# Kernel optimization log

Hardware: AMD Instinct MI355X
Metric: run time of the kernel (lower is better)

Reference implementation:

```python
import jax, jax.numpy as jnp
import numpy as np

TEMP = 0.7
ALPHA_ADV = 1.0
BETA_BAND = 0.5
BAND_L = 0.05
BAND_H = 0.2
W_HEUR = 0.5
W_LEAR = 0.5


def setup_inputs() -> dict:
    key = jax.random.key(0)
    ks = jax.random.split(key, 6)
    B, Sn, C, H, W = 2, 5, 64, 192, 192
    hid = 64
    return {
        "S": jax.random.normal(ks[0], (B, C, H, W), jnp.float32),
        "T": jax.random.normal(ks[1], (B, Sn, C, H, W), jnp.float32),
        "adapt_w": jax.random.normal(ks[2], (Sn, C, C), jnp.float32) / np.sqrt(C).astype(np.float32),
        "adapt_b": jnp.zeros((Sn, C), jnp.float32),
        "r_w1": jax.random.normal(ks[3], (hid, Sn * C * 3), jnp.float32) * 0.05,
        "r_b1": jnp.zeros((hid,), jnp.float32),
        "r_w2": jax.random.normal(ks[4], (Sn, hid), jnp.float32) * 0.05,
        "r_b2": jnp.zeros((Sn,), jnp.float32),
        "ema_mu": jnp.zeros((1, Sn, C, 1, 1), jnp.float32),
        "ema_sigma": jnp.ones((1, Sn, C, 1, 1), jnp.float32),
        "ema_proxy": jnp.zeros((1, Sn, 1, 1, 1), jnp.float32),
    }


def reference(S, T, adapt_w, adapt_b, r_w1, r_b1, r_w2, r_b2, ema_mu, ema_sigma, ema_proxy):
    B, Sn, C, H, W = T.shape
    bias = adapt_b[None, :, :, None, None]
    # per-sweep 1x1 conv == per-sweep channel matmul
    T_adapt = jnp.einsum('sdc,bschw->bsdhw', adapt_w, T) + bias          # [B,S,C,H,W]
    S_rep = jnp.einsum('sdc,bchw->bsdhw', adapt_w, S) + bias             # [B,S,C,H,W]
    Tz = (T_adapt - ema_mu) / ema_sigma
    Sz = (S_rep - ema_mu) / ema_sigma
    delta = Tz - Sz
    proxy = jnp.mean(delta * delta, axis=2, keepdims=True)               # [B,S,1,H,W]
    cur = jnp.mean(proxy, axis=(0, 3, 4), keepdims=True)                 # [1,S,1,1,1]
    # heuristic score (gamma_ucb = 0 -> no UCB term)
    impr = jax.lax.stop_gradient(ema_proxy - cur)
    adv = impr - jnp.mean(impr, axis=1, keepdims=True)
    below = jnp.maximum(BAND_L - cur, 0.0)
    above = jnp.maximum(cur - BAND_H, 0.0)
    band = -(below * below + above * above)
    score = ALPHA_ADV * adv + BETA_BAND * band                           # [1,S,1,1,1]
    score_heur = jnp.broadcast_to(score, proxy.shape)[:, :, 0]           # [B,S,H,W]
    # learned router: concat along channel of each sweep then 1x1 MLP
    x = jnp.concatenate([Sz, Tz, delta], axis=2).reshape(B, Sn * 3 * C, H, W)
    h = jax.nn.relu(jnp.einsum('oi,bihw->bohw', r_w1, x) + r_b1[None, :, None, None])
    score_learn = jnp.einsum('oi,bihw->bohw', r_w2, h) + r_b2[None, :, None, None]
    logits = W_HEUR * score_heur + W_LEAR * score_learn                  # [B,S,H,W]
    weights = jax.nn.softmax(logits / TEMP, axis=1)                      # soft gating over sweeps
    return weights
```

## Files before the change

### kernel.cpp

```cpp
#include <hip/hip_runtime.h>
#include <math.h>

#define HWSZ 36864
#define NTILE 576
#define NBLK 1152

typedef short bf16x8 __attribute__((ext_vector_type(8)));
typedef float f32x16 __attribute__((ext_vector_type(16)));
typedef unsigned int u32x4 __attribute__((ext_vector_type(4)));

__device__ __forceinline__ unsigned short f2bf(float x) {
    unsigned u = __float_as_uint(x);
    return (unsigned short)((u + 0x7fffu + ((u >> 16) & 1u)) >> 16);
}

__global__ void pre_dmat(const float* __restrict__ aw, const float* __restrict__ sigma,
                         float* __restrict__ Dmat) {
    int idx = blockIdx.x * 256 + threadIdx.x;
    if (idx < 20480) {
        int sd = idx >> 6;
        Dmat[idx] = aw[idx] / sigma[sd];
    }
}

__global__ void pre_weights(const float* __restrict__ rw1, const float* __restrict__ rb1,
                            const float* __restrict__ ab, const float* __restrict__ mu,
                            const float* __restrict__ sigma, const float* __restrict__ Dmat,
                            float* __restrict__ MT, float* __restrict__ MSp,
                            float* __restrict__ c1) {
    int idx = blockIdx.x * 256 + threadIdx.x;
    if (idx < 20480) {
        int s = idx / 4096, r = idx % 4096, o = r >> 6, c = r & 63;
        float sum = 0.f;
        const float* wp = rw1 + o * 960 + s * 192;
        const float* D  = Dmat + s * 4096 + c;
        #pragma unroll 8
        for (int d = 0; d < 64; ++d)
            sum = fmaf(wp[64 + d] + wp[128 + d], D[d * 64], sum);
        MT[idx] = sum;
    } else if (idx < 24576) {
        int k = idx - 20480;
        int o = k >> 6, c = k & 63;
        float sum = 0.f;
        for (int s = 0; s < 5; ++s) {
            const float* wp = rw1 + o * 960 + s * 192;
            const float* D  = Dmat + s * 4096 + c;
            #pragma unroll 8
            for (int d = 0; d < 64; ++d)
                sum = fmaf(wp[d] + wp[64 + d], D[d * 64], sum);
        }
        MSp[k] = sum;
    } else if (idx < 24640) {
        int o = idx - 24576;
        float sum = rb1[o];
        for (int s = 0; s < 5; ++s) {
            const float* wp = rw1 + o * 960 + s * 192;
            #pragma unroll 8
            for (int d = 0; d < 64; ++d) {
                int sd = s * 64 + d;
                sum = fmaf(wp[d] + wp[64 + d], (ab[sd] - mu[sd]) / sigma[sd], sum);
            }
        }
        c1[o] = sum;
    }
}

__global__ void pre_pack(const float* __restrict__ Dmat, const float* __restrict__ MT,
                         const float* __restrict__ MSp,
                         unsigned short* __restrict__ AfragW,
                         unsigned short* __restrict__ AfragSp) {
    int i = blockIdx.x * 256 + threadIdx.x;
    if (i < 40960) {
        int s = i / 8192, rem = i % 8192;
        int r = rem / 2048, rem2 = rem % 2048;
        int t = rem2 / 512, q = rem2 % 512;
        int l = q >> 3, e = q & 7;
        int R = 32 * r + (l & 31);
        int k = 16 * t + 8 * (l >> 5) + e;
        float v = (R < 64) ? Dmat[s * 4096 + R * 64 + k] : MT[s * 4096 + (R - 64) * 64 + k];
        AfragW[i] = f2bf(v);
    } else if (i < 45056) {
        int j = i - 40960;
        int r = j / 2048, rem2 = j % 2048;
        int t = rem2 / 512, q = rem2 % 512;
        int l = q >> 3, e = q & 7;
        float v = MSp[(32 * r + (l & 31)) * 64 + 16 * t + 8 * (l >> 5) + e];
        AfragSp[j] = f2bf(v);
    }
}

__global__ __launch_bounds__(256) void fused_main(
        const float* __restrict__ S, const float* __restrict__ T,
        const unsigned short* __restrict__ AfragW, const unsigned short* __restrict__ AfragSp,
        const float* __restrict__ c1, const float* __restrict__ rw2, const float* __restrict__ rb2,
        float* __restrict__ slearn, float* __restrict__ partial) {
    __shared__ __align__(16) unsigned short Xb[4096];
    __shared__ __align__(16) unsigned short Sb[4096];
    __shared__ float hbuf[64][64];
    __shared__ float wred[5][2];
    __shared__ float c1s[64];

    const int tid  = threadIdx.x;
    const int lane = tid & 63;
    const int w    = tid >> 6;
    const int blk  = blockIdx.x;
    const int b    = blk / NTILE;
    const int pix0 = (blk % NTILE) * 64;

    const int hi = lane >> 5;
    const int px = lane & 31;

    if (tid < 64) c1s[tid] = c1[tid];

    {
        const int pg = tid & 7, c0 = tid >> 3;
        for (int it = 0; it < 2; ++it) {
            int c = c0 + 32 * it;
            const float* Sp = S + ((size_t)(b * 64 + c)) * HWSZ + pix0 + pg * 8;
            float4 s0 = *(const float4*)Sp;
            float4 s1 = *(const float4*)(Sp + 4);
            u32x4 o;
            o.x = f2bf(s0.x) | ((unsigned)f2bf(s0.y) << 16);
            o.y = f2bf(s0.z) | ((unsigned)f2bf(s0.w) << 16);
            o.z = f2bf(s1.x) | ((unsigned)f2bf(s1.y) << 16);
            o.w = f2bf(s1.z) | ((unsigned)f2bf(s1.w) << 16);
            *(u32x4*)&Sb[c * 64 + pg * 8] = o;
        }
    }
    __syncthreads();

    auto stage_row = [&](int s, int c, int pg) {
        const float* Tp = T + ((size_t)((b * 5 + s) * 64 + c)) * HWSZ + pix0 + pg * 8;
        const float* Sp = S + ((size_t)(b * 64 + c)) * HWSZ + pix0 + pg * 8;
        float4 t0 = *(const float4*)Tp;
        float4 t1 = *(const float4*)(Tp + 4);
        float4 s0 = *(const float4*)Sp;
        float4 s1 = *(const float4*)(Sp + 4);
        u32x4 o;
        o.x = f2bf(t0.x - s0.x) | ((unsigned)f2bf(t0.y - s0.y) << 16);
        o.y = f2bf(t0.z - s0.z) | ((unsigned)f2bf(t0.w - s0.w) << 16);
        o.z = f2bf(t1.x - s1.x) | ((unsigned)f2bf(t1.y - s1.y) << 16);
        o.w = f2bf(t1.z - s1.z) | ((unsigned)f2bf(t1.w - s1.w) << 16);
        *(u32x4*)&Xb[c * 64 + pg * 8] = o;
    };

    auto run_gemm = [&](const unsigned short* afr, int fragblk, const unsigned short* lds,
                        f32x16& accA, f32x16& accB) {
        const bf16x8* ap = reinterpret_cast<const bf16x8*>(afr) + (size_t)fragblk * 256 + lane;
        bf16x8 Af[4];
        #pragma unroll
        for (int kt = 0; kt < 4; ++kt) Af[kt] = ap[kt * 64];
        #pragma unroll
        for (int kt = 0; kt < 4; ++kt) {
            bf16x8 Bq;
            int base = (kt * 16 + hi * 8) * 64 + px;
            #pragma unroll
            for (int e = 0; e < 8; ++e) Bq[e] = (short)lds[base + e * 64];
            accA = __builtin_amdgcn_mfma_f32_32x32x16_bf16(Af[kt], Bq, accA, 0, 0, 0);
        }
        #pragma unroll
        for (int kt = 0; kt < 4; ++kt) {
            bf16x8 Bq;
            int base = (kt * 16 + hi * 8) * 64 + px + 32;
            #pragma unroll
            for (int e = 0; e < 8; ++e) Bq[e] = (short)lds[base + e * 64];
            accB = __builtin_amdgcn_mfma_f32_32x32x16_bf16(Af[kt], Bq, accB, 0, 0, 0);
        }
    };

    f32x16 acc0, acc1;
    #pragma unroll
    for (int i = 0; i < 16; ++i) { acc0[i] = 0.f; acc1[i] = 0.f; }

    if (w < 2) {
        run_gemm(AfragSp, w, Sb, acc0, acc1);
        #pragma unroll
        for (int i = 0; i < 16; ++i) {
            int row = (i & 3) + 8 * (i >> 2) + 4 * hi + 32 * w;
            hbuf[row][px]      = acc0[i];
            hbuf[row][px + 32] = acc1[i];
        }
    } else {
        int t2 = tid - 128;
        int pg = t2 & 7, cb = t2 >> 3;
        for (int it = 0; it < 4; ++it) stage_row(0, cb + 16 * it, pg);
    }
    __syncthreads();

    for (int s = 0; s < 5; ++s) {
        if (w < 2) {
            #pragma unroll
            for (int i = 0; i < 16; ++i) { acc0[i] = 0.f; acc1[i] = 0.f; }
        }
        run_gemm(AfragW, s * 4 + w, Xb, acc0, acc1);
        if (w < 2) {
            float sq = 0.f;
            #pragma unroll
            for (int i = 0; i < 16; ++i) {
                sq = fmaf(acc0[i], acc0[i], sq);
                sq = fmaf(acc1[i], acc1[i], sq);
            }
            #pragma unroll
            for (int m = 1; m < 64; m <<= 1) sq += __shfl_xor(sq, m, 64);
            if (lane == 0) wred[s][w] = sq;
        }
        __syncthreads();
        if (s < 4) {
            int pg = tid & 7, c0 = tid >> 3;
            stage_row(s + 1, c0, pg);
            stage_row(s + 1, c0 + 32, pg);
            __syncthreads();
        }
    }

    if (w >= 2) {
        #pragma unroll
        for (int i = 0; i < 16; ++i) {
            int row = (i & 3) + 8 * (i >> 2) + 4 * hi + 32 * (w - 2);
            float v0 = hbuf[row][px]      + acc0[i] + c1s[row];
            float v1 = hbuf[row][px + 32] + acc1[i] + c1s[row];
            hbuf[row][px]      = fmaxf(v0, 0.f);
            hbuf[row][px + 32] = fmaxf(v1, 0.f);
        }
    }
    __syncthreads();

    {
        int p = tid & 63;
        for (int sp = w; sp < 5; sp += 4) {
            float sum = rb2[sp];
            #pragma unroll 8
            for (int o = 0; o < 64; ++o) sum = fmaf(rw2[sp * 64 + o], hbuf[o][p], sum);
            slearn[((size_t)(b * 5 + sp)) * HWSZ + pix0 + p] = sum;
        }
    }
    if (tid < 5) partial[blk * 5 + tid] = wred[tid][0] + wred[tid][1];
}

__global__ void score_kernel(const float* __restrict__ partial,
                             const float* __restrict__ ema_proxy,
                             float* __restrict__ scoreBuf) {
    __shared__ float red[256];
    __shared__ float cur[5];
    int tid = threadIdx.x;
    for (int s = 0; s < 5; ++s) {
        float sum = 0.f;
        for (int i = tid; i < NBLK; i += 256) sum += partial[i * 5 + s];
        red[tid] = sum;
        __syncthreads();
        for (int off = 128; off > 0; off >>= 1) {
            if (tid < off) red[tid] += red[tid + off];
            __syncthreads();
        }
        if (tid == 0) cur[s] = red[0] * (1.0f / (64.0f * 2.0f * HWSZ));
        __syncthreads();
    }
    if (tid == 0) {
        float impr[5]; float m = 0.f;
        for (int s = 0; s < 5; ++s) { impr[s] = ema_proxy[s] - cur[s]; m += impr[s]; }
        m *= 0.2f;
        for (int s = 0; s < 5; ++s) {
            float adv = impr[s] - m;
            float c = cur[s];
            float below = fmaxf(0.05f - c, 0.f);
            float above = fmaxf(c - 0.2f, 0.f);
            float band = -(below * below + above * above);
            scoreBuf[s] = 1.0f * adv + 0.5f * band;
        }
    }
}

__global__ void softmax_kernel(const float* __restrict__ slearn,
                               const float* __restrict__ scoreBuf,
                               float* __restrict__ out) {
    int i = blockIdx.x * 256 + threadIdx.x;
    if (i >= 2 * HWSZ) return;
    int b = i / HWSZ, p = i % HWSZ;
    float l[5];
    float mx = -1e30f;
    #pragma unroll
    for (int s = 0; s < 5; ++s) {
        float v = (0.5f * scoreBuf[s] + 0.5f * slearn[((size_t)(b * 5 + s)) * HWSZ + p]) / 0.7f;
        l[s] = v;
        mx = fmaxf(mx, v);
    }
    float sum = 0.f;
    #pragma unroll
    for (int s = 0; s < 5; ++s) { l[s] = expf(l[s] - mx); sum += l[s]; }
    float inv = 1.0f / sum;
    #pragma unroll
    for (int s = 0; s < 5; ++s) out[((size_t)(b * 5 + s)) * HWSZ + p] = l[s] * inv;
}

extern "C" void kernel_launch(void* const* d_in, const int* in_sizes, int n_in,
                              void* d_out, int out_size, void* d_ws, size_t ws_size,
                              hipStream_t stream) {
    const float* S   = (const float*)d_in[0];
    const float* T   = (const float*)d_in[1];
    const float* aw  = (const float*)d_in[2];
    const float* ab  = (const float*)d_in[3];
    const float* rw1 = (const float*)d_in[4];
    const float* rb1 = (const float*)d_in[5];
    const float* rw2 = (const float*)d_in[6];
    const float* rb2 = (const float*)d_in[7];
    const float* mu  = (const float*)d_in[8];
    const float* sg  = (const float*)d_in[9];
    const float* ep  = (const float*)d_in[10];

    float* ws = (float*)d_ws;
    float* c1f      = ws;
    float* scoreBuf = ws + 64;
    float* partial  = ws + 72;
    unsigned short* AfragW  = (unsigned short*)(ws + 5832);
    unsigned short* AfragSp = (unsigned short*)(ws + 26312);
    float* slearn   = ws + 28360;
    float* Dmat     = ws + 28360;
    float* MT       = ws + 48840;
    float* MSp      = ws + 69320;
    float* out = (float*)d_out;

    pre_dmat<<<80, 256, 0, stream>>>(aw, sg, Dmat);
    pre_weights<<<97, 256, 0, stream>>>(rw1, rb1, ab, mu, sg, Dmat, MT, MSp, c1f);
    pre_pack<<<176, 256, 0, stream>>>(Dmat, MT, MSp, AfragW, AfragSp);
    fused_main<<<NBLK, 256, 0, stream>>>(S, T, AfragW, AfragSp, c1f, rw2, rb2, slearn, partial);
    score_kernel<<<1, 256, 0, stream>>>(partial, ep, scoreBuf);
    softmax_kernel<<<288, 256, 0, stream>>>(slearn, scoreBuf, out);
}
```

Baseline: 69.29 us.

## Restructure fused kernel: 128-pixel tiles, register-prefetched T, double-buffered LDS, register MLP

Each block now covers 128 pixels instead of 64, so half as many blocks are launched. Each wave owns a 32-pixel column and runs both the delta and hidden GEMMs for all four M-tiles, which keeps the hidden accumulators in registers across sweeps. S is read once and kept in registers as bf16, while the next sweep's T is prefetched into registers and written to an alternating LDS buffer with an XOR swizzle, removing one barrier per sweep and the repeated S reloads. The final 64-to-5 projection is done from registers with a cross-half shuffle instead of through an LDS hidden buffer. The cost is higher register pressure, fewer blocks for occupancy, and S being rounded to bf16 before the subtraction.

```diff
diff --git a/kernel.cpp b/kernel.cpp
--- a/kernel.cpp
+++ b/kernel.cpp
@@ -2,8 +2,9 @@
 #include <math.h>
 
 #define HWSZ 36864
-#define NTILE 576
-#define NBLK 1152
+#define NPIX 128
+#define NT2  288
+#define NBLK2 576
 
 typedef short bf16x8 __attribute__((ext_vector_type(8)));
 typedef float f32x16 __attribute__((ext_vector_type(16)));
@@ -94,147 +95,195 @@
         const unsigned short* __restrict__ AfragW, const unsigned short* __restrict__ AfragSp,
         const float* __restrict__ c1, const float* __restrict__ rw2, const float* __restrict__ rb2,
         float* __restrict__ slearn, float* __restrict__ partial) {
-    __shared__ __align__(16) unsigned short Xb[4096];
-    __shared__ __align__(16) unsigned short Sb[4096];
-    __shared__ float hbuf[64][64];
-    __shared__ float wred[5][2];
+    __shared__ __align__(16) unsigned short bufA[8192];
+    __shared__ __align__(16) unsigned short bufB[8192];
+    __shared__ float w2s[320];
     __shared__ float c1s[64];
+    __shared__ float rb2s[8];
+    __shared__ float wred[5][4];
 
     const int tid  = threadIdx.x;
     const int lane = tid & 63;
     const int w    = tid >> 6;
+    const int hi   = lane >> 5;
+    const int px   = lane & 31;
+    const int col  = (w << 5) + px;
+
     const int blk  = blockIdx.x;
-    const int b    = blk / NTILE;
-    const int pix0 = (blk % NTILE) * 64;
-
-    const int hi = lane >> 5;
-    const int px = lane & 31;
-
+    const int b    = blk / NT2;
+    const int pix0 = (blk % NT2) * NPIX;
+
+    for (int i = tid; i < 320; i += 256) w2s[i] = rw2[i];
     if (tid < 64) c1s[tid] = c1[tid];
+    if (tid < 5)  rb2s[tid] = rb2[tid];
+
+    const int pg = tid & 7;
+    const int c0 = tid >> 3;
+    const float* Sbase = S + ((size_t)b * 64) * HWSZ + pix0 + pg * 16;
+    const float* Tbase = T + ((size_t)(b * 5) * 64) * HWSZ + pix0 + pg * 16;
+
+    float4 sldr[8];
+    #pragma unroll
+    for (int r = 0; r < 2; ++r) {
+        const float* p = Sbase + (size_t)(c0 + 32 * r) * HWSZ;
+        #pragma unroll
+        for (int j = 0; j < 4; ++j) sldr[r * 4 + j] = *(const float4*)(p + 4 * j);
+    }
+    float4 tr[8];
+    #pragma unroll
+    for (int r = 0; r < 2; ++r) {
+        const float* p = Tbase + (size_t)(c0 + 32 * r) * HWSZ;
+        #pragma unroll
+        for (int j = 0; j < 4; ++j) tr[r * 4 + j] = *(const float4*)(p + 4 * j);
+    }
+
+    u32x4 sreg[4];
+    #pragma unroll
+    for (int r = 0; r < 2; ++r) {
+        const float4* v = sldr + 4 * r;
+        unsigned o[8];
+        #pragma unroll
+        for (int q = 0; q < 4; ++q) {
+            o[2 * q]     = (unsigned)f2bf(v[q].x) | ((unsigned)f2bf(v[q].y) << 16);
+            o[2 * q + 1] = (unsigned)f2bf(v[q].z) | ((unsigned)f2bf(v[q].w) << 16);
+        }
+        u32x4 o0, o1;
+        o0.x = o[0]; o0.y = o[1]; o0.z = o[2]; o0.w = o[3];
+        o1.x = o[4]; o1.y = o[5]; o1.z = o[6]; o1.w = o[7];
+        sreg[2 * r] = o0; sreg[2 * r + 1] = o1;
+        int c = c0 + 32 * r;
+        int flip = (c & 8) ? 32 : 0;
+        unsigned short* dst = &bufA[c * 128 + ((pg * 16) ^ flip)];
+        *(u32x4*)dst = o0;
+        *(u32x4*)(dst + 8) = o1;
+    }
+    __syncthreads();
+
+    auto writeX = [&](unsigned short* buf) {
+        #pragma unroll
+        for (int r = 0; r < 2; ++r) {
+            const float4* t = tr + 4 * r;
+            float f[16];
+            #pragma unroll
+            for (int q = 0; q < 4; ++q) {
+                f[4 * q] = t[q].x; f[4 * q + 1] = t[q].y;
+                f[4 * q + 2] = t[q].z; f[4 * q + 3] = t[q].w;
+            }
+            unsigned spv[8];
+            spv[0] = sreg[2 * r].x; spv[1] = sreg[2 * r].y; spv[2] = sreg[2 * r].z; spv[3] = sreg[2 * r].w;
+            spv[4] = sreg[2 * r + 1].x; spv[5] = sreg[2 * r + 1].y; spv[6] = sreg[2 * r + 1].z; spv[7] = sreg[2 * r + 1].w;
+            unsigned o[8];
+            #pragma unroll
+            for (int k = 0; k < 8; ++k) {
+                float slo = __uint_as_float(spv[k] << 16);
+                float shi = __uint_as_float(spv[k] & 0xffff0000u);
+                unsigned short xlo = f2bf(f[2 * k] - slo);
+                unsigned short xhi = f2bf(f[2 * k + 1] - shi);
+                o[k] = (unsigned)xlo | ((unsigned)xhi << 16);
+            }
+            u32x4 o0, o1;
+            o0.x = o[0]; o0.y = o[1]; o0.z = o[2]; o0.w = o[3];
+            o1.x = o[4]; o1.y = o[5]; o1.z = o[6]; o1.w = o[7];
+            int c = c0 + 32 * r;
+            int flip = (c & 8) ? 32 : 0;
+            unsigned short* dst = &buf[c * 128 + ((pg * 16) ^ flip)];
+            *(u32x4*)dst = o0;
+            *(u32x4*)(dst + 8) = o1;
+        }
+    };
+    auto loadT = [&](int s) {
+        #pragma unroll
+        for (int r = 0; r < 2; ++r) {
+            const float* p = Tbase + (size_t)(s * 64 + c0 + 32 * r) * HWSZ;
+            #pragma unroll
+            for (int j = 0; j < 4; ++j) tr[r * 4 + j] = *(const float4*)(p + 4 * j);
+        }
+    };
+
+    f32x16 h0, h1;
+    #pragma unroll
+    for (int i = 0; i < 16; ++i) { h0[i] = 0.f; h1[i] = 0.f; }
 
     {
-        const int pg = tid & 7, c0 = tid >> 3;
-        for (int it = 0; it < 2; ++it) {
-            int c = c0 + 32 * it;
-            const float* Sp = S + ((size_t)(b * 64 + c)) * HWSZ + pix0 + pg * 8;
-            float4 s0 = *(const float4*)Sp;
-            float4 s1 = *(const float4*)(Sp + 4);
-            u32x4 o;
-            o.x = f2bf(s0.x) | ((unsigned)f2bf(s0.y) << 16);
-            o.y = f2bf(s0.z) | ((unsigned)f2bf(s0.w) << 16);
-            o.z = f2bf(s1.x) | ((unsigned)f2bf(s1.y) << 16);
-            o.w = f2bf(s1.z) | ((unsigned)f2bf(s1.w) << 16);
-            *(u32x4*)&Sb[c * 64 + pg * 8] = o;
-        }
-    }
+        const bf16x8* ap = (const bf16x8*)AfragSp + lane;
+        #pragma unroll
+        for (int kt = 0; kt < 4; ++kt) {
+            int k0 = kt * 16 + hi * 8;
+            int flip = hi ? 32 : 0;
+            const unsigned short* bp = &bufA[k0 * 128 + (col ^ flip)];
+            bf16x8 Bq;
+            #pragma unroll
+            for (int e = 0; e < 8; ++e) Bq[e] = (short)bp[e * 128];
+            h0 = __builtin_amdgcn_mfma_f32_32x32x16_bf16(ap[(0 * 4 + kt) * 64], Bq, h0, 0, 0, 0);
+            h1 = __builtin_amdgcn_mfma_f32_32x32x16_bf16(ap[(1 * 4 + kt) * 64], Bq, h1, 0, 0, 0);
+        }
+    }
+    writeX(bufB);
+    loadT(1);
     __syncthreads();
 
-    auto stage_row = [&](int s, int c, int pg) {
-        const float* Tp = T + ((size_t)((b * 5 + s) * 64 + c)) * HWSZ + pix0 + pg * 8;
-        const float* Sp = S + ((size_t)(b * 64 + c)) * HWSZ + pix0 + pg * 8;
-        float4 t0 = *(const float4*)Tp;
-        float4 t1 = *(const float4*)(Tp + 4);
-        float4 s0 = *(const float4*)Sp;
-        float4 s1 = *(const float4*)(Sp + 4);
-        u32x4 o;
-        o.x = f2bf(t0.x - s0.x) | ((unsigned)f2bf(t0.y - s0.y) << 16);
-        o.y = f2bf(t0.z - s0.z) | ((unsigned)f2bf(t0.w - s0.w) << 16);
-        o.z = f2bf(t1.x - s1.x) | ((unsigned)f2bf(t1.y - s1.y) << 16);
-        o.w = f2bf(t1.z - s1.z) | ((unsigned)f2bf(t1.w - s1.w) << 16);
-        *(u32x4*)&Xb[c * 64 + pg * 8] = o;
-    };
-
-    auto run_gemm = [&](const unsigned short* afr, int fragblk, const unsigned short* lds,
-                        f32x16& accA, f32x16& accB) {
-        const bf16x8* ap = reinterpret_cast<const bf16x8*>(afr) + (size_t)fragblk * 256 + lane;
-        bf16x8 Af[4];
-        #pragma unroll
-        for (int kt = 0; kt < 4; ++kt) Af[kt] = ap[kt * 64];
+    #pragma unroll
+    for (int s = 0; s < 5; ++s) {
+        const unsigned short* cur = (s & 1) ? bufA : bufB;
+        unsigned short* nxt       = (s & 1) ? bufB : bufA;
+        const bf16x8* ap = (const bf16x8*)AfragW + (size_t)(s * 16) * 64 + lane;
+
+        f32x16 d0, d1;
+        #pragma unroll
+        for (int i = 0; i < 16; ++i) { d0[i] = 0.f; d1[i] = 0.f; }
+
         #pragma unroll
         for (int kt = 0; kt < 4; ++kt) {
+            int k0 = kt * 16 + hi * 8;
+            int flip = hi ? 32 : 0;
+            const unsigned short* bp = &cur[k0 * 128 + (col ^ flip)];
             bf16x8 Bq;
-            int base = (kt * 16 + hi * 8) * 64 + px;
-            #pragma unroll
-            for (int e = 0; e < 8; ++e) Bq[e] = (short)lds[base + e * 64];
-            accA = __builtin_amdgcn_mfma_f32_32x32x16_bf16(Af[kt], Bq, accA, 0, 0, 0);
-        }
-        #pragma unroll
-        for (int kt = 0; kt < 4; ++kt) {
-            bf16x8 Bq;
-            int base = (kt * 16 + hi * 8) * 64 + px + 32;
-            #pragma unroll
-            for (int e = 0; e < 8; ++e) Bq[e] = (short)lds[base + e * 64];
-            accB = __builtin_amdgcn_mfma_f32_32x32x16_bf16(Af[kt], Bq, accB, 0, 0, 0);
-        }
-    };
-
-    f32x16 acc0, acc1;
-    #pragma unroll
-    for (int i = 0; i < 16; ++i) { acc0[i] = 0.f; acc1[i] = 0.f; }
-
-    if (w < 2) {
-        run_gemm(AfragSp, w, Sb, acc0, acc1);
+            #pragma unroll
+            for (int e = 0; e < 8; ++e) Bq[e] = (short)bp[e * 128];
+            d0 = __builtin_amdgcn_mfma_f32_32x32x16_bf16(ap[(0 * 4 + kt) * 64], Bq, d0, 0, 0, 0);
+            d1 = __builtin_amdgcn_mfma_f32_32x32x16_bf16(ap[(1 * 4 + kt) * 64], Bq, d1, 0, 0, 0);
+            h0 = __builtin_amdgcn_mfma_f32_32x32x16_bf16(ap[(2 * 4 + kt) * 64], Bq, h0, 0, 0, 0);
+            h1 = __builtin_amdgcn_mfma_f32_32x32x16_bf16(ap[(3 * 4 + kt) * 64], Bq, h1, 0, 0, 0);
+        }
+        float sq = 0.f;
         #pragma unroll
         for (int i = 0; i < 16; ++i) {
-            int row = (i & 3) + 8 * (i >> 2) + 4 * hi + 32 * w;
-            hbuf[row][px]      = acc0[i];
-            hbuf[row][px + 32] = acc1[i];
-        }
-    } else {
-        int t2 = tid - 128;
-        int pg = t2 & 7, cb = t2 >> 3;
-        for (int it = 0; it < 4; ++it) stage_row(0, cb + 16 * it, pg);
-    }
-    __syncthreads();
-
-    for (int s = 0; s < 5; ++s) {
-        if (w < 2) {
-            #pragma unroll
-            for (int i = 0; i < 16; ++i) { acc0[i] = 0.f; acc1[i] = 0.f; }
-        }
-        run_gemm(AfragW, s * 4 + w, Xb, acc0, acc1);
-        if (w < 2) {
-            float sq = 0.f;
-            #pragma unroll
-            for (int i = 0; i < 16; ++i) {
-                sq = fmaf(acc0[i], acc0[i], sq);
-                sq = fmaf(acc1[i], acc1[i], sq);
-            }
-            #pragma unroll
-            for (int m = 1; m < 64; m <<= 1) sq += __shfl_xor(sq, m, 64);
-            if (lane == 0) wred[s][w] = sq;
+            sq = fmaf(d0[i], d0[i], sq);
+            sq = fmaf(d1[i], d1[i], sq);
+        }
+        #pragma unroll
+        for (int m = 1; m < 64; m <<= 1) sq += __shfl_xor(sq, m, 64);
+        if (lane == 0) wred[s][w] = sq;
+
+        if (s < 4) {
+            writeX(nxt);
+            if (s < 3) loadT(s + 2);
         }
         __syncthreads();
-        if (s < 4) {
-            int pg = tid & 7, c0 = tid >> 3;
-            stage_row(s + 1, c0, pg);
-            stage_row(s + 1, c0 + 32, pg);
-            __syncthreads();
-        }
-    }
-
-    if (w >= 2) {
+    }
+
+    if (tid < 5)
+        partial[blk * 5 + tid] = wred[tid][0] + wred[tid][1] + wred[tid][2] + wred[tid][3];
+
+    #pragma unroll
+    for (int i = 0; i < 16; ++i) {
+        int row0 = (i & 3) + 8 * (i >> 2) + 4 * hi;
+        h0[i] = fmaxf(h0[i] + c1s[row0], 0.f);
+        h1[i] = fmaxf(h1[i] + c1s[row0 + 32], 0.f);
+    }
+    #pragma unroll
+    for (int sp = 0; sp < 5; ++sp) {
+        float acc = 0.f;
         #pragma unroll
         for (int i = 0; i < 16; ++i) {
-            int row = (i & 3) + 8 * (i >> 2) + 4 * hi + 32 * (w - 2);
-            float v0 = hbuf[row][px]      + acc0[i] + c1s[row];
-            float v1 = hbuf[row][px + 32] + acc1[i] + c1s[row];
-            hbuf[row][px]      = fmaxf(v0, 0.f);
-            hbuf[row][px + 32] = fmaxf(v1, 0.f);
-        }
-    }
-    __syncthreads();
-
-    {
-        int p = tid & 63;
-        for (int sp = w; sp < 5; sp += 4) {
-            float sum = rb2[sp];
-            #pragma unroll 8
-            for (int o = 0; o < 64; ++o) sum = fmaf(rw2[sp * 64 + o], hbuf[o][p], sum);
-            slearn[((size_t)(b * 5 + sp)) * HWSZ + pix0 + p] = sum;
-        }
-    }
-    if (tid < 5) partial[blk * 5 + tid] = wred[tid][0] + wred[tid][1];
+            int row0 = (i & 3) + 8 * (i >> 2) + 4 * hi;
+            acc = fmaf(w2s[sp * 64 + row0], h0[i], acc);
+            acc = fmaf(w2s[sp * 64 + row0 + 32], h1[i], acc);
+        }
+        acc += __shfl_xor(acc, 32, 64);
+        if (lane < 32)
+            slearn[((size_t)(b * 5 + sp)) * HWSZ + pix0 + col] = acc + rb2s[sp];
+    }
 }
 
 __global__ void score_kernel(const float* __restrict__ partial,
@@ -245,7 +294,7 @@
     int tid = threadIdx.x;
     for (int s = 0; s < 5; ++s) {
         float sum = 0.f;
-        for (int i = tid; i < NBLK; i += 256) sum += partial[i * 5 + s];
+        for (int i = tid; i < NBLK2; i += 256) sum += partial[i * 5 + s];
         red[tid] = sum;
         __syncthreads();
         for (int off = 128; off > 0; off >>= 1) {
@@ -322,7 +371,7 @@
     pre_dmat<<<80, 256, 0, stream>>>(aw, sg, Dmat);
     pre_weights<<<97, 256, 0, stream>>>(rw1, rb1, ab, mu, sg, Dmat, MT, MSp, c1f);
     pre_pack<<<176, 256, 0, stream>>>(Dmat, MT, MSp, AfragW, AfragSp);
-    fused_main<<<NBLK, 256, 0, stream>>>(S, T, AfragW, AfragSp, c1f, rw2, rb2, slearn, partial);
+    fused_main<<<NBLK2, 256, 0, stream>>>(S, T, AfragW, AfragSp, c1f, rw2, rb2, slearn, partial);
     score_kernel<<<1, 256, 0, stream>>>(partial, ep, scoreBuf);
     softmax_kernel<<<288, 256, 0, stream>>>(slearn, scoreBuf, out);
 }
```

Result: slower. 78.58 us (+13.4%).

## Restructure fused kernel into single-wave 32-pixel tiles with register-resident operands

Applied to the files above, without the earlier changes.

The main kernel now uses one 64-thread wave per 32-pixel tile instead of a 256-thread block per 64-pixel tile. S and T are loaded straight from global memory into registers as MFMA B-operands, replacing the LDS staging buffers and block barriers. The hidden layer stays in accumulators, and the second layer is reduced with a shuffle. T loads for the next sweep are software-pipelined against the current GEMM, and pre_dmat is fused into pre_weights to remove a launch. The cost is strided scalar global loads with 32-pixel coalescing instead of float4 loads, higher register pressure, and twice as many partial sums.

```diff
diff --git a/kernel.cpp b/kernel.cpp
--- a/kernel.cpp
+++ b/kernel.cpp
@@ -2,8 +2,8 @@
 #include <math.h>
 
 #define HWSZ 36864
-#define NTILE 576
-#define NBLK 1152
+#define NWID 2304
+#define PXW  32
 
 typedef short bf16x8 __attribute__((ext_vector_type(8)));
 typedef float f32x16 __attribute__((ext_vector_type(16)));
@@ -14,29 +14,22 @@
     return (unsigned short)((u + 0x7fffu + ((u >> 16) & 1u)) >> 16);
 }
 
-__global__ void pre_dmat(const float* __restrict__ aw, const float* __restrict__ sigma,
-                         float* __restrict__ Dmat) {
+__global__ void pre_weights(const float* __restrict__ rw1, const float* __restrict__ rb1,
+                            const float* __restrict__ aw, const float* __restrict__ ab,
+                            const float* __restrict__ mu, const float* __restrict__ sg,
+                            float* __restrict__ Dmat, float* __restrict__ MT,
+                            float* __restrict__ MSp, float* __restrict__ c1) {
     int idx = blockIdx.x * 256 + threadIdx.x;
     if (idx < 20480) {
-        int sd = idx >> 6;
-        Dmat[idx] = aw[idx] / sigma[sd];
-    }
-}
-
-__global__ void pre_weights(const float* __restrict__ rw1, const float* __restrict__ rb1,
-                            const float* __restrict__ ab, const float* __restrict__ mu,
-                            const float* __restrict__ sigma, const float* __restrict__ Dmat,
-                            float* __restrict__ MT, float* __restrict__ MSp,
-                            float* __restrict__ c1) {
-    int idx = blockIdx.x * 256 + threadIdx.x;
-    if (idx < 20480) {
+        Dmat[idx] = aw[idx] / sg[idx >> 6];
         int s = idx / 4096, r = idx % 4096, o = r >> 6, c = r & 63;
         float sum = 0.f;
         const float* wp = rw1 + o * 960 + s * 192;
-        const float* D  = Dmat + s * 4096 + c;
+        const float* A  = aw + s * 4096 + c;
+        const float* G  = sg + s * 64;
         #pragma unroll 8
         for (int d = 0; d < 64; ++d)
-            sum = fmaf(wp[64 + d] + wp[128 + d], D[d * 64], sum);
+            sum = fmaf(wp[64 + d] + wp[128 + d], A[d * 64] / G[d], sum);
         MT[idx] = sum;
     } else if (idx < 24576) {
         int k = idx - 20480;
@@ -44,10 +37,11 @@
         float sum = 0.f;
         for (int s = 0; s < 5; ++s) {
             const float* wp = rw1 + o * 960 + s * 192;
-            const float* D  = Dmat + s * 4096 + c;
+            const float* A  = aw + s * 4096 + c;
+            const float* G  = sg + s * 64;
             #pragma unroll 8
             for (int d = 0; d < 64; ++d)
-                sum = fmaf(wp[d] + wp[64 + d], D[d * 64], sum);
+                sum = fmaf(wp[d] + wp[64 + d], A[d * 64] / G[d], sum);
         }
         MSp[k] = sum;
     } else if (idx < 24640) {
@@ -58,7 +52,7 @@
             #pragma unroll 8
             for (int d = 0; d < 64; ++d) {
                 int sd = s * 64 + d;
-                sum = fmaf(wp[d] + wp[64 + d], (ab[sd] - mu[sd]) / sigma[sd], sum);
+                sum = fmaf(wp[d] + wp[64 + d], (ab[sd] - mu[sd]) / sg[sd], sum);
             }
         }
         c1[o] = sum;
@@ -89,152 +83,131 @@
     }
 }
 
-__global__ __launch_bounds__(256) void fused_main(
+__global__ __launch_bounds__(64, 2) void fused_main(
         const float* __restrict__ S, const float* __restrict__ T,
         const unsigned short* __restrict__ AfragW, const unsigned short* __restrict__ AfragSp,
         const float* __restrict__ c1, const float* __restrict__ rw2, const float* __restrict__ rb2,
         float* __restrict__ slearn, float* __restrict__ partial) {
-    __shared__ __align__(16) unsigned short Xb[4096];
-    __shared__ __align__(16) unsigned short Sb[4096];
-    __shared__ float hbuf[64][64];
-    __shared__ float wred[5][2];
+    __shared__ float w2s[320];
     __shared__ float c1s[64];
-
-    const int tid  = threadIdx.x;
-    const int lane = tid & 63;
-    const int w    = tid >> 6;
-    const int blk  = blockIdx.x;
-    const int b    = blk / NTILE;
-    const int pix0 = (blk % NTILE) * 64;
-
-    const int hi = lane >> 5;
-    const int px = lane & 31;
-
-    if (tid < 64) c1s[tid] = c1[tid];
+    __shared__ float rb2s[8];
+
+    const int lane = threadIdx.x;
+    const int hi = lane >> 5, px = lane & 31;
+    const int wid = blockIdx.x;
+    const int b = wid / 1152;
+    const int pix0 = (wid % 1152) * PXW;
+
+    for (int i = lane; i < 320; i += 64) w2s[i] = rw2[i];
+    c1s[lane] = c1[lane];
+    if (lane < 5) rb2s[lane] = rb2[lane];
+    __syncthreads();
+
+    const float* Sb = S + ((size_t)b * 64 + hi * 8) * HWSZ + pix0 + px;
+    const float* Tb = T + ((size_t)(b * 5 * 64) + hi * 8) * HWSZ + pix0 + px;
+
+    float sv[32];
+    #pragma unroll
+    for (int i = 0; i < 32; ++i)
+        sv[i] = Sb[(size_t)((i >> 3) * 16 + (i & 7)) * HWSZ];
+    bf16x8 sf[4];
+    #pragma unroll
+    for (int kt = 0; kt < 4; ++kt) {
+        union { bf16x8 h; u32x4 u; } U;
+        #pragma unroll
+        for (int j = 0; j < 4; ++j)
+            U.u[j] = (unsigned)f2bf(sv[kt * 8 + 2 * j]) |
+                     ((unsigned)f2bf(sv[kt * 8 + 2 * j + 1]) << 16);
+        sf[kt] = U.h;
+    }
+
+    auto loadT = [&](float* tv, int s) {
+        const float* p = Tb + (size_t)s * 64 * HWSZ;
+        #pragma unroll
+        for (int i = 0; i < 32; ++i)
+            tv[i] = p[(size_t)((i >> 3) * 16 + (i & 7)) * HWSZ];
+    };
+    auto packX = [&](const float* tv, bf16x8* xf) {
+        #pragma unroll
+        for (int kt = 0; kt < 4; ++kt) {
+            union { bf16x8 h; u32x4 u; } sU, xU;
+            sU.h = sf[kt];
+            #pragma unroll
+            for (int j = 0; j < 4; ++j) {
+                float slo = __uint_as_float(sU.u[j] << 16);
+                float shi = __uint_as_float(sU.u[j] & 0xffff0000u);
+                xU.u[j] = (unsigned)f2bf(tv[kt * 8 + 2 * j] - slo) |
+                          ((unsigned)f2bf(tv[kt * 8 + 2 * j + 1] - shi) << 16);
+            }
+            xf[kt] = xU.h;
+        }
+    };
+
+    f32x16 h0, h1;
+    #pragma unroll
+    for (int i = 0; i < 16; ++i) { h0[i] = 0.f; h1[i] = 0.f; }
+
+    float tvA[32], tvB[32];
+    loadT(tvA, 0);
 
     {
-        const int pg = tid & 7, c0 = tid >> 3;
-        for (int it = 0; it < 2; ++it) {
-            int c = c0 + 32 * it;
-            const float* Sp = S + ((size_t)(b * 64 + c)) * HWSZ + pix0 + pg * 8;
-            float4 s0 = *(const float4*)Sp;
-            float4 s1 = *(const float4*)(Sp + 4);
-            u32x4 o;
-            o.x = f2bf(s0.x) | ((unsigned)f2bf(s0.y) << 16);
-            o.y = f2bf(s0.z) | ((unsigned)f2bf(s0.w) << 16);
-            o.z = f2bf(s1.x) | ((unsigned)f2bf(s1.y) << 16);
-            o.w = f2bf(s1.z) | ((unsigned)f2bf(s1.w) << 16);
-            *(u32x4*)&Sb[c * 64 + pg * 8] = o;
-        }
-    }
-    __syncthreads();
-
-    auto stage_row = [&](int s, int c, int pg) {
-        const float* Tp = T + ((size_t)((b * 5 + s) * 64 + c)) * HWSZ + pix0 + pg * 8;
-        const float* Sp = S + ((size_t)(b * 64 + c)) * HWSZ + pix0 + pg * 8;
-        float4 t0 = *(const float4*)Tp;
-        float4 t1 = *(const float4*)(Tp + 4);
-        float4 s0 = *(const float4*)Sp;
-        float4 s1 = *(const float4*)(Sp + 4);
-        u32x4 o;
-        o.x = f2bf(t0.x - s0.x) | ((unsigned)f2bf(t0.y - s0.y) << 16);
-        o.y = f2bf(t0.z - s0.z) | ((unsigned)f2bf(t0.w - s0.w) << 16);
-        o.z = f2bf(t1.x - s1.x) | ((unsigned)f2bf(t1.y - s1.y) << 16);
-        o.w = f2bf(t1.z - s1.z) | ((unsigned)f2bf(t1.w - s1.w) << 16);
-        *(u32x4*)&Xb[c * 64 + pg * 8] = o;
+        const bf16x8* asp = (const bf16x8*)AfragSp + lane;
+        #pragma unroll
+        for (int kt = 0; kt < 4; ++kt) {
+            h0 = __builtin_amdgcn_mfma_f32_32x32x16_bf16(asp[kt * 64],       sf[kt], h0, 0, 0, 0);
+            h1 = __builtin_amdgcn_mfma_f32_32x32x16_bf16(asp[(4 + kt) * 64], sf[kt], h1, 0, 0, 0);
+        }
+    }
+
+    auto gemmS = [&](int s, const bf16x8* xf) {
+        const bf16x8* aw = (const bf16x8*)AfragW + (size_t)s * 16 * 64 + lane;
+        f32x16 d0, d1;
+        #pragma unroll
+        for (int i = 0; i < 16; ++i) { d0[i] = 0.f; d1[i] = 0.f; }
+        #pragma unroll
+        for (int kt = 0; kt < 4; ++kt) {
+            d0 = __builtin_amdgcn_mfma_f32_32x32x16_bf16(aw[(0 * 4 + kt) * 64], xf[kt], d0, 0, 0, 0);
+            d1 = __builtin_amdgcn_mfma_f32_32x32x16_bf16(aw[(1 * 4 + kt) * 64], xf[kt], d1, 0, 0, 0);
+            h0 = __builtin_amdgcn_mfma_f32_32x32x16_bf16(aw[(2 * 4 + kt) * 64], xf[kt], h0, 0, 0, 0);
+            h1 = __builtin_amdgcn_mfma_f32_32x32x16_bf16(aw[(3 * 4 + kt) * 64], xf[kt], h1, 0, 0, 0);
+        }
+        float sq = 0.f;
+        #pragma unroll
+        for (int i = 0; i < 16; ++i) {
+            sq = fmaf(d0[i], d0[i], sq);
+            sq = fmaf(d1[i], d1[i], sq);
+        }
+        #pragma unroll
+        for (int m = 1; m < 64; m <<= 1) sq += __shfl_xor(sq, m, 64);
+        if (lane == 0) partial[wid * 5 + s] = sq;
     };
 
-    auto run_gemm = [&](const unsigned short* afr, int fragblk, const unsigned short* lds,
-                        f32x16& accA, f32x16& accB) {
-        const bf16x8* ap = reinterpret_cast<const bf16x8*>(afr) + (size_t)fragblk * 256 + lane;
-        bf16x8 Af[4];
-        #pragma unroll
-        for (int kt = 0; kt < 4; ++kt) Af[kt] = ap[kt * 64];
-        #pragma unroll
-        for (int kt = 0; kt < 4; ++kt) {
-            bf16x8 Bq;
-            int base = (kt * 16 + hi * 8) * 64 + px;
-            #pragma unroll
-            for (int e = 0; e < 8; ++e) Bq[e] = (short)lds[base + e * 64];
-            accA = __builtin_amdgcn_mfma_f32_32x32x16_bf16(Af[kt], Bq, accA, 0, 0, 0);
-        }
-        #pragma unroll
-        for (int kt = 0; kt < 4; ++kt) {
-            bf16x8 Bq;
-            int base = (kt * 16 + hi * 8) * 64 + px + 32;
-            #pragma unroll
-            for (int e = 0; e < 8; ++e) Bq[e] = (short)lds[base + e * 64];
-            accB = __builtin_amdgcn_mfma_f32_32x32x16_bf16(Af[kt], Bq, accB, 0, 0, 0);
-        }
-    };
-
-    f32x16 acc0, acc1;
-    #pragma unroll
-    for (int i = 0; i < 16; ++i) { acc0[i] = 0.f; acc1[i] = 0.f; }
-
-    if (w < 2) {
-        run_gemm(AfragSp, w, Sb, acc0, acc1);
+    bf16x8 xf[4];
+    packX(tvA, xf); loadT(tvB, 1); gemmS(0, xf);
+    packX(tvB, xf); loadT(tvA, 2); gemmS(1, xf);
+    packX(tvA, xf); loadT(tvB, 3); gemmS(2, xf);
+    packX(tvB, xf); loadT(tvA, 4); gemmS(3, xf);
+    packX(tvA, xf);                gemmS(4, xf);
+
+    #pragma unroll
+    for (int i = 0; i < 16; ++i) {
+        int row0 = (i & 3) + 8 * (i >> 2) + 4 * hi;
+        h0[i] = fmaxf(h0[i] + c1s[row0], 0.f);
+        h1[i] = fmaxf(h1[i] + c1s[row0 + 32], 0.f);
+    }
+    #pragma unroll
+    for (int sp = 0; sp < 5; ++sp) {
+        float acc = 0.f;
         #pragma unroll
         for (int i = 0; i < 16; ++i) {
-            int row = (i & 3) + 8 * (i >> 2) + 4 * hi + 32 * w;
-            hbuf[row][px]      = acc0[i];
-            hbuf[row][px + 32] = acc1[i];
-        }
-    } else {
-        int t2 = tid - 128;
-        int pg = t2 & 7, cb = t2 >> 3;
-        for (int it = 0; it < 4; ++it) stage_row(0, cb + 16 * it, pg);
-    }
-    __syncthreads();
-
-    for (int s = 0; s < 5; ++s) {
-        if (w < 2) {
-            #pragma unroll
-            for (int i = 0; i < 16; ++i) { acc0[i] = 0.f; acc1[i] = 0.f; }
-        }
-        run_gemm(AfragW, s * 4 + w, Xb, acc0, acc1);
-        if (w < 2) {
-            float sq = 0.f;
-            #pragma unroll
-            for (int i = 0; i < 16; ++i) {
-                sq = fmaf(acc0[i], acc0[i], sq);
-                sq = fmaf(acc1[i], acc1[i], sq);
-            }
-            #pragma unroll
-            for (int m = 1; m < 64; m <<= 1) sq += __shfl_xor(sq, m, 64);
-            if (lane == 0) wred[s][w] = sq;
-        }
-        __syncthreads();
-        if (s < 4) {
-            int pg = tid & 7, c0 = tid >> 3;
-            stage_row(s + 1, c0, pg);
-            stage_row(s + 1, c0 + 32, pg);
-            __syncthreads();
-        }
-    }
-
-    if (w >= 2) {
-        #pragma unroll
-        for (int i = 0; i < 16; ++i) {
-            int row = (i & 3) + 8 * (i >> 2) + 4 * hi + 32 * (w - 2);
-            float v0 = hbuf[row][px]      + acc0[i] + c1s[row];
-            float v1 = hbuf[row][px + 32] + acc1[i] + c1s[row];
-            hbuf[row][px]      = fmaxf(v0, 0.f);
-            hbuf[row][px + 32] = fmaxf(v1, 0.f);
-        }
-    }
-    __syncthreads();
-
-    {
-        int p = tid & 63;
-        for (int sp = w; sp < 5; sp += 4) {
-            float sum = rb2[sp];
-            #pragma unroll 8
-            for (int o = 0; o < 64; ++o) sum = fmaf(rw2[sp * 64 + o], hbuf[o][p], sum);
-            slearn[((size_t)(b * 5 + sp)) * HWSZ + pix0 + p] = sum;
-        }
-    }
-    if (tid < 5) partial[blk * 5 + tid] = wred[tid][0] + wred[tid][1];
+            int row0 = (i & 3) + 8 * (i >> 2) + 4 * hi;
+            acc = fmaf(w2s[sp * 64 + row0],      h0[i], acc);
+            acc = fmaf(w2s[sp * 64 + row0 + 32], h1[i], acc);
+        }
+        acc += __shfl_xor(acc, 32, 64);
+        if (lane < 32)
+            slearn[((size_t)(b * 5 + sp)) * HWSZ + pix0 + px] = acc + rb2s[sp];
+    }
 }
 
 __global__ void score_kernel(const float* __restrict__ partial,
@@ -245,7 +218,7 @@
     int tid = threadIdx.x;
     for (int s = 0; s < 5; ++s) {
         float sum = 0.f;
-        for (int i = tid; i < NBLK; i += 256) sum += partial[i * 5 + s];
+        for (int i = tid; i < NWID; i += 256) sum += partial[i * 5 + s];
         red[tid] = sum;
         __syncthreads();
         for (int off = 128; off > 0; off >>= 1) {
@@ -311,18 +284,17 @@
     float* c1f      = ws;
     float* scoreBuf = ws + 64;
     float* partial  = ws + 72;
-    unsigned short* AfragW  = (unsigned short*)(ws + 5832);
-    unsigned short* AfragSp = (unsigned short*)(ws + 26312);
-    float* slearn   = ws + 28360;
-    float* Dmat     = ws + 28360;
-    float* MT       = ws + 48840;
-    float* MSp      = ws + 69320;
+    unsigned short* AfragW  = (unsigned short*)(ws + 11592);
+    unsigned short* AfragSp = (unsigned short*)(ws + 32072);
+    float* slearn   = ws + 34120;
+    float* Dmat     = ws + 34120;
+    float* MT       = ws + 54600;
+    float* MSp      = ws + 75080;
     float* out = (float*)d_out;
 
-    pre_dmat<<<80, 256, 0, stream>>>(aw, sg, Dmat);
-    pre_weights<<<97, 256, 0, stream>>>(rw1, rb1, ab, mu, sg, Dmat, MT, MSp, c1f);
+    pre_weights<<<97, 256, 0, stream>>>(rw1, rb1, aw, ab, mu, sg, Dmat, MT, MSp, c1f);
     pre_pack<<<176, 256, 0, stream>>>(Dmat, MT, MSp, AfragW, AfragSp);
-    fused_main<<<NBLK, 256, 0, stream>>>(S, T, AfragW, AfragSp, c1f, rw2, rb2, slearn, partial);
+    fused_main<<<NWID, 64, 0, stream>>>(S, T, AfragW, AfragSp, c1f, rw2, rb2, slearn, partial);
     score_kernel<<<1, 256, 0, stream>>>(partial, ep, scoreBuf);
     softmax_kernel<<<288, 256, 0, stream>>>(slearn, scoreBuf, out);
 }
```

Result: slower. 71.28 us (+2.9%).
